# Performance work log

Measured on AMD Instinct MI355X. Metric: run time of the kernel, lower is better.

Reference implementation:

```python
import jax, jax.numpy as jnp
import numpy as np

B, T, D, U = 32, 1024, 512, 512

def hard_sigmoid(x):
    # Keras hard_sigmoid: clip(0.2*x + 0.5, 0, 1)
    return jnp.clip(x * 0.2 + 0.5, 0.0, 1.0)

def setup_inputs() -> dict:
    key = jax.random.key(0)
    k1, k2, k3 = jax.random.split(key, 3)
    x = jax.random.normal(k1, (B, T, D), dtype=jnp.float32)
    kernel = jax.random.normal(k2, (D, 4 * U), dtype=jnp.float32) * 0.02
    recurrent_kernel = jax.random.normal(k3, (U, 4 * U), dtype=jnp.float32) * 0.02
    # unit_forget_bias: forget-gate slice initialized to 1
    bias = jnp.zeros((4 * U,), dtype=jnp.float32).at[U:2 * U].set(1.0)
    return {"x": x, "kernel": kernel, "recurrent_kernel": recurrent_kernel, "bias": bias}

def reference(x, kernel, recurrent_kernel, bias):
    units = recurrent_kernel.shape[0]
    batch = x.shape[0]
    # Precompute input projections for all timesteps in one big GEMM
    # (implementation=2 style): [B, T, 4U]
    xz = jnp.einsum('btd,dg->btg', x, kernel) + bias
    xz_t = jnp.transpose(xz, (1, 0, 2))  # [T, B, 4U]

    h0 = jnp.zeros((batch, units), dtype=x.dtype)
    c0 = jnp.zeros((batch, units), dtype=x.dtype)

    def step(carry, z_x):
        h, c = carry
        z = z_x + h @ recurrent_kernel  # [B, 4U]
        zi, zf, zc, zo = jnp.split(z, 4, axis=-1)
        i = hard_sigmoid(zi)
        f = hard_sigmoid(zf)
        c_new = f * c + i * jnp.tanh(zc)
        o = hard_sigmoid(zo)
        h_new = o * jnp.tanh(c_new)
        return (h_new, c_new), h_new

    (_, _), hs = jax.lax.scan(step, (h0, c0), xz_t)  # hs: [T, B, U]
    return jnp.transpose(hs, (1, 0, 2))  # [B, T, U] (return_sequences=True)
```

## Files before the change

### kernel.cpp

```cpp
#include <hip/hip_runtime.h>


#define TT 1024
#define DD 512
#define UU 512
#define NCOL 2048
#define SENT 0xFFFFFFFFu
#define RDEPTH 4
#define SLOTS 4
#define WS_NEED 279552

typedef float f32x2 __attribute__((ext_vector_type(2)));
typedef float f32x4 __attribute__((ext_vector_type(4)));

__device__ __forceinline__ float hsig(float v) {
  return fminf(fmaxf(0.2f * v + 0.5f, 0.0f), 1.0f);
}
__device__ __forceinline__ float tanh_fast(float x) {
  float e = __expf(2.0f * x);
  return 1.0f - 2.0f / (e + 1.0f);
}

template <bool SLEEP>
__device__ __forceinline__ void wavebar(int* ctr, int& ep) {
  asm volatile("s_waitcnt lgkmcnt(0)" ::: "memory");
  if ((threadIdx.x & 63) == 0)
    __hip_atomic_fetch_add(ctr, 1, __ATOMIC_RELAXED, __HIP_MEMORY_SCOPE_WORKGROUP);
  ep += 4;
  while (__hip_atomic_load(ctr, __ATOMIC_RELAXED, __HIP_MEMORY_SCOPE_WORKGROUP) < ep) {
    if (SLEEP) __builtin_amdgcn_s_sleep(1);
  }
  asm volatile("" ::: "memory");
}

#define SENTSHOT(v0,v1,v2,v3,v4,v5,v6,v7,p0,p1,p2,p3)                    \
  asm volatile(                                                          \
      "global_load_dword %0, %8, off sc0 sc1\n\t"                        \
      "global_load_dword %1, %8, off offset:256 sc0 sc1\n\t"             \
      "global_load_dword %2, %9, off sc0 sc1\n\t"                        \
      "global_load_dword %3, %9, off offset:256 sc0 sc1\n\t"             \
      "global_load_dword %4, %10, off sc0 sc1\n\t"                       \
      "global_load_dword %5, %10, off offset:256 sc0 sc1\n\t"            \
      "global_load_dword %6, %11, off sc0 sc1\n\t"                       \
      "global_load_dword %7, %11, off offset:256 sc0 sc1\n\t"            \
      "s_waitcnt vmcnt(0)"                                               \
      : "=v"(v0), "=v"(v1), "=v"(v2), "=v"(v3),                          \
        "=v"(v4), "=v"(v5), "=v"(v6), "=v"(v7)                           \
      : "v"(p0), "v"(p1), "v"(p2), "v"(p3)                               \
      : "memory")

#define OK8(v0,v1,v2,v3,v4,v5,v6,v7)                                     \
  ((v0 != SENT) & (v1 != SENT) & (v2 != SENT) & (v3 != SENT) &           \
   (v4 != SENT) & (v5 != SENT) & (v6 != SENT) & (v7 != SENT))

__global__ __launch_bounds__(512, 2) void lstm_persistent(
    const float* __restrict__ x,
    const float* __restrict__ Wk,
    const float* __restrict__ Wr,
    const float* __restrict__ bias,
    float* __restrict__ out,
    int* __restrict__ wsbase) {
  const int tid = (int)threadIdx.x;
  const int g   = (int)blockIdx.x & 7;
  const int w   = (int)blockIdx.x >> 3;
  const bool crit = (tid < 256);
  const int l   = tid & 63;
  const bool has_ws = (wsbase != nullptr);

  int* tags   = wsbase;
  int* wscnt  = wsbase + 4096;
  int* wsmask = wsbase + 4104;
  float* fastH = (float*)wsbase + 4352;

  if (has_ws && tid == 0) {
    unsigned xcd;
    asm volatile("s_getreg_b32 %0, hwreg(HW_REG_XCC_ID)" : "=s"(xcd));
    __hip_atomic_fetch_or(wsmask + g, 1u << (xcd & 31), __ATOMIC_RELAXED,
                          __HIP_MEMORY_SCOPE_AGENT);
    __hip_atomic_fetch_add(wscnt + g, 1, __ATOMIC_RELEASE,
                           __HIP_MEMORY_SCOPE_AGENT);
  }

  __shared__ float LX[8][4][65];
  __shared__ float LR[2][8][4][66];
  __shared__ float RING[RDEPTH][4][66];
  __shared__ float LH[4][8][68];
  __shared__ float LB[64];
  __shared__ int cXZdone, cCRITdone, cXZbar, cCRITbar, sFast;

  if (tid == 0) { cXZdone = 0; cCRITdone = 0; cXZbar = 0; cCRITbar = 0; }
  if (tid < 64) LB[tid] = bias[(tid >> 4) * UU + w * 16 + (tid & 15)];

  f32x2 W2[64];
  {
    const int wv  = tid >> 6;
    const int idx = tid & 255;
    const int cp  = crit ? (l & 31) : (idx & 31);
    const int ko  = crit ? (2 * (wv & 3) + (l >> 5)) : (idx >> 5);
    const int gcb = (cp >> 3) * UU + w * 16 + ((2 * cp) & 15);
    const float* M = crit ? Wr : Wk;
#pragma unroll
    for (int j = 0; j < 64; ++j)
      W2[j] = *(const f32x2*)(M + (size_t)(64 * ko + j) * NCOL + gcb);
  }
  if (tid == 0) {
    int fast = 0;
    if (has_ws) {
      int ok = 0;
      for (int it = 0; it < 200000; ++it) {
        if (__hip_atomic_load(wscnt + g, __ATOMIC_ACQUIRE,
                              __HIP_MEMORY_SCOPE_AGENT) >= 32) { ok = 1; break; }
        __builtin_amdgcn_s_sleep(8);
      }
      if (ok) {
        unsigned m = (unsigned)__hip_atomic_load(wsmask + g, __ATOMIC_RELAXED,
                                                 __HIP_MEMORY_SCOPE_AGENT);
        fast = (__popc(m) == 1) ? 1 : 0;
      }
    }
    sFast = fast;
  }
  __syncthreads();
  const bool fastm = (sFast != 0);

  if (crit) {
    const int wv  = tid >> 6;
    const int kq0 = 2 * wv;
    const int kql = kq0 + (l >> 5);
    const int cp  = l & 31;
    const unsigned* ou0 = (const unsigned*)out + (size_t)(g * 4 + 0) * TT * UU;
    const unsigned* ou1 = (const unsigned*)out + (size_t)(g * 4 + 1) * TT * UU;
    const unsigned* ou2 = (const unsigned*)out + (size_t)(g * 4 + 2) * TT * UU;
    const unsigned* ou3 = (const unsigned*)out + (size_t)(g * 4 + 3) * TT * UU;
    float c_state = 0.0f;
    int epC = 0;

    for (int t = 0; t < TT; ++t) {
      if (t > 0) {
        const size_t roff = (size_t)(t - 1) * UU + 128 * wv + l;
        const unsigned* p0 = ou0 + roff;
        const unsigned* p1 = ou1 + roff;
        const unsigned* p2 = ou2 + roff;
        const unsigned* p3 = ou3 + roff;
        unsigned v0, v1, v2, v3, v4, v5, v6, v7;
        if (fastm) {
          const int slot = (t - 1) & (SLOTS - 1);
          const int* tp = tags +
              (((g * SLOTS + slot) * 32) + 8 * wv + (l & 7)) * 4 + ((l >> 3) & 3);
          const float* fb0 = fastH + ((size_t)((g * SLOTS + slot) * 4 + 0)) * 512 + 128 * wv + l;
          const float* fb1 = fastH + ((size_t)((g * SLOTS + slot) * 4 + 1)) * 512 + 128 * wv + l;
          const float* fb2 = fastH + ((size_t)((g * SLOTS + slot) * 4 + 2)) * 512 + 128 * wv + l;
          const float* fb3 = fastH + ((size_t)((g * SLOTS + slot) * 4 + 3)) * 512 + 128 * wv + l;
          int miss = 0;
          for (;;) {
            int tg;
            asm volatile("global_load_dword %0, %1, off sc0\n\ts_waitcnt vmcnt(0)"
                         : "=v"(tg) : "v"(tp) : "memory");
            if (__all(tg == t - 1)) {
              asm volatile(
                  "global_load_dword %0, %8, off sc0\n\t"
                  "global_load_dword %1, %8, off offset:256 sc0\n\t"
                  "global_load_dword %2, %9, off sc0\n\t"
                  "global_load_dword %3, %9, off offset:256 sc0\n\t"
                  "global_load_dword %4, %10, off sc0\n\t"
                  "global_load_dword %5, %10, off offset:256 sc0\n\t"
                  "global_load_dword %6, %11, off sc0\n\t"
                  "global_load_dword %7, %11, off offset:256 sc0\n\t"
                  "s_waitcnt vmcnt(0)"
                  : "=v"(v0), "=v"(v1), "=v"(v2), "=v"(v3),
                    "=v"(v4), "=v"(v5), "=v"(v6), "=v"(v7)
                  : "v"(fb0), "v"(fb1), "v"(fb2), "v"(fb3)
                  : "memory");
              break;
            }
            if (((++miss) & 7) == 0) {
              SENTSHOT(v0, v1, v2, v3, v4, v5, v6, v7, p0, p1, p2, p3);
              if (__all(OK8(v0, v1, v2, v3, v4, v5, v6, v7))) break;
            }
            __builtin_amdgcn_s_sleep(1);
          }
        } else {
          for (;;) {
            SENTSHOT(v0, v1, v2, v3, v4, v5, v6, v7, p0, p1, p2, p3);
            if (__all(OK8(v0, v1, v2, v3, v4, v5, v6, v7))) break;
            __builtin_amdgcn_s_sleep(16);
          }
        }
        LH[0][kq0    ][l] = __uint_as_float(v0);
        LH[0][kq0 + 1][l] = __uint_as_float(v1);
        LH[1][kq0    ][l] = __uint_as_float(v2);
        LH[1][kq0 + 1][l] = __uint_as_float(v3);
        LH[2][kq0    ][l] = __uint_as_float(v4);
        LH[2][kq0 + 1][l] = __uint_as_float(v5);
        LH[3][kq0    ][l] = __uint_as_float(v6);
        LH[3][kq0 + 1][l] = __uint_as_float(v7);
        asm volatile("s_waitcnt lgkmcnt(0)" ::: "memory");
        __builtin_amdgcn_sched_barrier(0);
        __builtin_amdgcn_s_setprio(1);
        f32x2 a0 = {0.f, 0.f}, a1 = {0.f, 0.f}, a2 = {0.f, 0.f}, a3 = {0.f, 0.f};
#pragma unroll
        for (int j4 = 0; j4 < 16; ++j4) {
          f32x4 h0 = *(const f32x4*)&LH[0][kql][4 * j4];
          f32x4 h1 = *(const f32x4*)&LH[1][kql][4 * j4];
          f32x4 h2 = *(const f32x4*)&LH[2][kql][4 * j4];
          f32x4 h3 = *(const f32x4*)&LH[3][kql][4 * j4];
#pragma unroll
          for (int jj = 0; jj < 4; ++jj) {
            f32x2 wj = W2[4 * j4 + jj];
            a0 += (f32x2){h0[jj], h0[jj]} * wj;
            a1 += (f32x2){h1[jj], h1[jj]} * wj;
            a2 += (f32x2){h2[jj], h2[jj]} * wj;
            a3 += (f32x2){h3[jj], h3[jj]} * wj;
          }
        }
        __builtin_amdgcn_s_setprio(0);
        const int p = t & 1;
        *(f32x2*)&LR[p][kql][0][2 * cp] = a0;
        *(f32x2*)&LR[p][kql][1][2 * cp] = a1;
        *(f32x2*)&LR[p][kql][2][2 * cp] = a2;
        *(f32x2*)&LR[p][kql][3][2 * cp] = a3;
      }
      float s0 = 0.f, s1 = 0.f, s2 = 0.f, s3 = 0.f;
      if (l < 16) {
        while (__hip_atomic_load(&cXZdone, __ATOMIC_RELAXED,
                                 __HIP_MEMORY_SCOPE_WORKGROUP) < t + 1) {
        }
        asm volatile("" ::: "memory");
        const int ss = t & (RDEPTH - 1);
        s0 = RING[ss][wv][l +  0] + LB[l +  0];
        s1 = RING[ss][wv][l + 16] + LB[l + 16];
        s2 = RING[ss][wv][l + 32] + LB[l + 32];
        s3 = RING[ss][wv][l + 48] + LB[l + 48];
      }
      wavebar<false>(&cCRITbar, epC);
      if (l == 0)
        __hip_atomic_fetch_add(&cCRITdone, 1, __ATOMIC_RELAXED,
                               __HIP_MEMORY_SCOPE_WORKGROUP);
      if (l < 16) {
        if (t > 0) {
          const int p = t & 1;
#pragma unroll
          for (int kq = 0; kq < 8; ++kq) {
            s0 += LR[p][kq][wv][l +  0];
            s1 += LR[p][kq][wv][l + 16];
            s2 += LR[p][kq][wv][l + 32];
            s3 += LR[p][kq][wv][l + 48];
          }
        }
        float gi = hsig(s0);
        float gf = hsig(s1);
        float gc = tanh_fast(s2);
        float go = hsig(s3);
        c_state = gf * c_state + gi * gc;
        float h = go * tanh_fast(c_state);
        if (fastm) {
          float* fp = fastH +
              ((size_t)((g * SLOTS + (t & (SLOTS - 1))) * 4 + wv)) * 512 + 16 * w + l;
          asm volatile("global_store_dword %0, %1, off sc0"
                       :: "v"(fp), "v"(h) : "memory");
          asm volatile("s_waitcnt vmcnt(0)" ::: "memory");
          if (l == 0) {
            int tv = t;
            int* tq = tags + (((g * SLOTS + (t & (SLOTS - 1))) * 32) + w) * 4 + wv;
            asm volatile("global_store_dword %0, %1, off sc0"
                         :: "v"(tq), "v"(tv) : "memory");
          }
        }
        __hip_atomic_store(
            out + ((size_t)(g * 4 + wv) * TT + t) * UU + w * 16 + l, h,
            __ATOMIC_RELAXED, __HIP_MEMORY_SCOPE_AGENT);
      }
    }
  } else {
    const int idx = tid & 255;
    const int o   = idx >> 5;
    const int cp  = idx & 31;
    const float* xb0 = x + (size_t)(g * 4 + 0) * TT * DD + o * 64;
    const float* xb1 = x + (size_t)(g * 4 + 1) * TT * DD + o * 64;
    const float* xb2 = x + (size_t)(g * 4 + 2) * TT * DD + o * 64;
    const float* xb3 = x + (size_t)(g * 4 + 3) * TT * DD + o * 64;
    int epX = 0;

    for (int t = 0; t < TT; ++t) {
      const size_t off = (size_t)t * DD;
      f32x2 a0 = {0.f, 0.f}, a1 = {0.f, 0.f}, a2 = {0.f, 0.f}, a3 = {0.f, 0.f};
#pragma unroll
      for (int j4 = 0; j4 < 16; ++j4) {
        f32x4 v0 = *(const f32x4*)(xb0 + off + 4 * j4);
        f32x4 v1 = *(const f32x4*)(xb1 + off + 4 * j4);
        f32x4 v2 = *(const f32x4*)(xb2 + off + 4 * j4);
        f32x4 v3 = *(const f32x4*)(xb3 + off + 4 * j4);
#pragma unroll
        for (int jj = 0; jj < 4; ++jj) {
          f32x2 wj = W2[4 * j4 + jj];
          a0 += (f32x2){v0[jj], v0[jj]} * wj;
          a1 += (f32x2){v1[jj], v1[jj]} * wj;
          a2 += (f32x2){v2[jj], v2[jj]} * wj;
          a3 += (f32x2){v3[jj], v3[jj]} * wj;
        }
      }
      *(f32x2*)&LX[o][0][2 * cp] = a0;
      *(f32x2*)&LX[o][1][2 * cp] = a1;
      *(f32x2*)&LX[o][2][2 * cp] = a2;
      *(f32x2*)&LX[o][3][2 * cp] = a3;
      wavebar<true>(&cXZbar, epX);
      if (t >= RDEPTH) {
        while (__hip_atomic_load(&cCRITdone, __ATOMIC_RELAXED,
                                 __HIP_MEMORY_SCOPE_WORKGROUP) <
               4 * (t - RDEPTH + 1)) {
          __builtin_amdgcn_s_sleep(1);
        }
        asm volatile("" ::: "memory");
      }
      {
        const int b2 = idx >> 6, c3 = idx & 63;
        float ssum = 0.f;
#pragma unroll
        for (int oo = 0; oo < 8; ++oo) ssum += LX[oo][b2][c3];
        RING[t & (RDEPTH - 1)][b2][c3] = ssum;
      }
      wavebar<true>(&cXZbar, epX);
      if (idx == 0) {
        asm volatile("s_waitcnt lgkmcnt(0)" ::: "memory");
        __hip_atomic_fetch_add(&cXZdone, 1, __ATOMIC_RELAXED,
                               __HIP_MEMORY_SCOPE_WORKGROUP);
      }
    }
  }
}

extern "C" void kernel_launch(void* const* d_in, const int* in_sizes, int n_in,
                              void* d_out, int out_size, void* d_ws, size_t ws_size,
                              hipStream_t stream) {
  const float* x    = (const float*)d_in[0];
  const float* Wk   = (const float*)d_in[1];
  const float* Wr   = (const float*)d_in[2];
  const float* bias = (const float*)d_in[3];
  float* out = (float*)d_out;

  int* wsbase = nullptr;
  if (ws_size >= (size_t)WS_NEED) {
    wsbase = (int*)d_ws;
    hipMemsetAsync(wsbase, 0xFF, 16384, stream);
    hipMemsetAsync((char*)d_ws + 16384, 0x00, 64, stream);
  }
  hipMemsetAsync(out, 0xFF, (size_t)out_size * sizeof(float), stream);
  lstm_persistent<<<256, 512, 0, stream>>>(x, Wk, Wr, bias, out, wsbase);
}
```

Baseline: 4.561 ms.

## Encode step parity into hidden-state values to drop separate tag flags

Replaces the tag-plus-data handshake for the fast hidden-state exchange with self-validating data. Each h value is stored offset by ±3, with the sign chosen by the step's colour bit, so the reader checks exponent and sign to confirm freshness and then subtracts the offset. This removes the tag store, the vmcnt wait before it, and the separate tag poll round-trip on the critical recurrence path. It adds a small rounding error from the ±3 add and subtract, relies on |h|<1 to keep the encoded exponent in range, and drops the ordering between data and tag writes.

```diff
diff --git a/kernel.cpp b/kernel.cpp
--- a/kernel.cpp
+++ b/kernel.cpp
@@ -7,8 +7,7 @@
 #define NCOL 2048
 #define SENT 0xFFFFFFFFu
 #define RDEPTH 4
-#define SLOTS 4
-#define WS_NEED 279552
+#define WS_NEED 263168
 
 typedef float f32x2 __attribute__((ext_vector_type(2)));
 typedef float f32x4 __attribute__((ext_vector_type(4)));
@@ -53,6 +52,11 @@
   ((v0 != SENT) & (v1 != SENT) & (v2 != SENT) & (v3 != SENT) &           \
    (v4 != SENT) & (v5 != SENT) & (v6 != SENT) & (v7 != SENT))
 
+__device__ __forceinline__ int encok(unsigned b, unsigned expsign) {
+  unsigned e = (b >> 23) & 0xFF;
+  return (int)(((e == 128u) | (e == 129u)) & ((b >> 31) == expsign));
+}
+
 __global__ __launch_bounds__(512, 2) void lstm_persistent(
     const float* __restrict__ x,
     const float* __restrict__ Wk,
@@ -67,10 +71,9 @@
   const int l   = tid & 63;
   const bool has_ws = (wsbase != nullptr);
 
-  int* tags   = wsbase;
-  int* wscnt  = wsbase + 4096;
-  int* wsmask = wsbase + 4104;
-  float* fastH = (float*)wsbase + 4352;
+  int* wscnt  = wsbase;
+  int* wsmask = wsbase + 8;
+  float* ring = (float*)wsbase + 256;
 
   if (has_ws && tid == 0) {
     unsigned xcd;
@@ -143,39 +146,65 @@
         const unsigned* p2 = ou2 + roff;
         const unsigned* p3 = ou3 + roff;
         unsigned v0, v1, v2, v3, v4, v5, v6, v7;
+        float h0v, h1v, h2v, h3v, h4v, h5v, h6v, h7v;
         if (fastm) {
-          const int slot = (t - 1) & (SLOTS - 1);
-          const int* tp = tags +
-              (((g * SLOTS + slot) * 32) + 8 * wv + (l & 7)) * 4 + ((l >> 3) & 3);
-          const float* fb0 = fastH + ((size_t)((g * SLOTS + slot) * 4 + 0)) * 512 + 128 * wv + l;
-          const float* fb1 = fastH + ((size_t)((g * SLOTS + slot) * 4 + 1)) * 512 + 128 * wv + l;
-          const float* fb2 = fastH + ((size_t)((g * SLOTS + slot) * 4 + 2)) * 512 + 128 * wv + l;
-          const float* fb3 = fastH + ((size_t)((g * SLOTS + slot) * 4 + 3)) * 512 + 128 * wv + l;
+          const int tau   = t - 1;
+          const int slot  = tau & 3;
+          const unsigned color = (unsigned)((tau >> 2) & 1);
+          const unsigned expsign = color ? 0u : 1u;
+          const float dec = color ? -3.0f : 3.0f;
+          const unsigned* fb0 = (const unsigned*)ring +
+              ((size_t)((g * 4 + slot) * 4 + 0)) * 512 + 128 * wv + l;
+          const unsigned* fb1 = (const unsigned*)ring +
+              ((size_t)((g * 4 + slot) * 4 + 1)) * 512 + 128 * wv + l;
+          const unsigned* fb2 = (const unsigned*)ring +
+              ((size_t)((g * 4 + slot) * 4 + 2)) * 512 + 128 * wv + l;
+          const unsigned* fb3 = (const unsigned*)ring +
+              ((size_t)((g * 4 + slot) * 4 + 3)) * 512 + 128 * wv + l;
           int miss = 0;
           for (;;) {
-            int tg;
-            asm volatile("global_load_dword %0, %1, off sc0\n\ts_waitcnt vmcnt(0)"
-                         : "=v"(tg) : "v"(tp) : "memory");
-            if (__all(tg == t - 1)) {
-              asm volatile(
-                  "global_load_dword %0, %8, off sc0\n\t"
-                  "global_load_dword %1, %8, off offset:256 sc0\n\t"
-                  "global_load_dword %2, %9, off sc0\n\t"
-                  "global_load_dword %3, %9, off offset:256 sc0\n\t"
-                  "global_load_dword %4, %10, off sc0\n\t"
-                  "global_load_dword %5, %10, off offset:256 sc0\n\t"
-                  "global_load_dword %6, %11, off sc0\n\t"
-                  "global_load_dword %7, %11, off offset:256 sc0\n\t"
-                  "s_waitcnt vmcnt(0)"
-                  : "=v"(v0), "=v"(v1), "=v"(v2), "=v"(v3),
-                    "=v"(v4), "=v"(v5), "=v"(v6), "=v"(v7)
-                  : "v"(fb0), "v"(fb1), "v"(fb2), "v"(fb3)
-                  : "memory");
+            asm volatile(
+                "global_load_dword %0, %8, off sc0\n\t"
+                "global_load_dword %1, %8, off offset:256 sc0\n\t"
+                "global_load_dword %2, %9, off sc0\n\t"
+                "global_load_dword %3, %9, off offset:256 sc0\n\t"
+                "global_load_dword %4, %10, off sc0\n\t"
+                "global_load_dword %5, %10, off offset:256 sc0\n\t"
+                "global_load_dword %6, %11, off sc0\n\t"
+                "global_load_dword %7, %11, off offset:256 sc0\n\t"
+                "s_waitcnt vmcnt(0)"
+                : "=v"(v0), "=v"(v1), "=v"(v2), "=v"(v3),
+                  "=v"(v4), "=v"(v5), "=v"(v6), "=v"(v7)
+                : "v"(fb0), "v"(fb1), "v"(fb2), "v"(fb3)
+                : "memory");
+            int ok = encok(v0, expsign) & encok(v1, expsign) &
+                     encok(v2, expsign) & encok(v3, expsign) &
+                     encok(v4, expsign) & encok(v5, expsign) &
+                     encok(v6, expsign) & encok(v7, expsign);
+            if (__all(ok)) {
+              h0v = __uint_as_float(v0) + dec;
+              h1v = __uint_as_float(v1) + dec;
+              h2v = __uint_as_float(v2) + dec;
+              h3v = __uint_as_float(v3) + dec;
+              h4v = __uint_as_float(v4) + dec;
+              h5v = __uint_as_float(v5) + dec;
+              h6v = __uint_as_float(v6) + dec;
+              h7v = __uint_as_float(v7) + dec;
               break;
             }
             if (((++miss) & 7) == 0) {
               SENTSHOT(v0, v1, v2, v3, v4, v5, v6, v7, p0, p1, p2, p3);
-              if (__all(OK8(v0, v1, v2, v3, v4, v5, v6, v7))) break;
+              if (__all(OK8(v0, v1, v2, v3, v4, v5, v6, v7))) {
+                h0v = __uint_as_float(v0);
+                h1v = __uint_as_float(v1);
+                h2v = __uint_as_float(v2);
+                h3v = __uint_as_float(v3);
+                h4v = __uint_as_float(v4);
+                h5v = __uint_as_float(v5);
+                h6v = __uint_as_float(v6);
+                h7v = __uint_as_float(v7);
+                break;
+              }
             }
             __builtin_amdgcn_s_sleep(1);
           }
@@ -185,15 +214,23 @@
             if (__all(OK8(v0, v1, v2, v3, v4, v5, v6, v7))) break;
             __builtin_amdgcn_s_sleep(16);
           }
-        }
-        LH[0][kq0    ][l] = __uint_as_float(v0);
-        LH[0][kq0 + 1][l] = __uint_as_float(v1);
-        LH[1][kq0    ][l] = __uint_as_float(v2);
-        LH[1][kq0 + 1][l] = __uint_as_float(v3);
-        LH[2][kq0    ][l] = __uint_as_float(v4);
-        LH[2][kq0 + 1][l] = __uint_as_float(v5);
-        LH[3][kq0    ][l] = __uint_as_float(v6);
-        LH[3][kq0 + 1][l] = __uint_as_float(v7);
+          h0v = __uint_as_float(v0);
+          h1v = __uint_as_float(v1);
+          h2v = __uint_as_float(v2);
+          h3v = __uint_as_float(v3);
+          h4v = __uint_as_float(v4);
+          h5v = __uint_as_float(v5);
+          h6v = __uint_as_float(v6);
+          h7v = __uint_as_float(v7);
+        }
+        LH[0][kq0    ][l] = h0v;
+        LH[0][kq0 + 1][l] = h1v;
+        LH[1][kq0    ][l] = h2v;
+        LH[1][kq0 + 1][l] = h3v;
+        LH[2][kq0    ][l] = h4v;
+        LH[2][kq0 + 1][l] = h5v;
+        LH[3][kq0    ][l] = h6v;
+        LH[3][kq0 + 1][l] = h7v;
         asm volatile("s_waitcnt lgkmcnt(0)" ::: "memory");
         __builtin_amdgcn_sched_barrier(0);
         __builtin_amdgcn_s_setprio(1);
@@ -254,17 +291,11 @@
         c_state = gf * c_state + gi * gc;
         float h = go * tanh_fast(c_state);
         if (fastm) {
-          float* fp = fastH +
-              ((size_t)((g * SLOTS + (t & (SLOTS - 1))) * 4 + wv)) * 512 + 16 * w + l;
+          const float enc = ((t >> 2) & 1) ? (h + 3.0f) : (h - 3.0f);
+          float* fp = ring +
+              ((size_t)((g * 4 + (t & 3)) * 4 + wv)) * 512 + 16 * w + l;
           asm volatile("global_store_dword %0, %1, off sc0"
-                       :: "v"(fp), "v"(h) : "memory");
-          asm volatile("s_waitcnt vmcnt(0)" ::: "memory");
-          if (l == 0) {
-            int tv = t;
-            int* tq = tags + (((g * SLOTS + (t & (SLOTS - 1))) * 32) + w) * 4 + wv;
-            asm volatile("global_store_dword %0, %1, off sc0"
-                         :: "v"(tq), "v"(tv) : "memory");
-          }
+                       :: "v"(fp), "v"(enc) : "memory");
         }
         __hip_atomic_store(
             out + ((size_t)(g * 4 + wv) * TT + t) * UU + w * 16 + l, h,
@@ -341,8 +372,8 @@
   int* wsbase = nullptr;
   if (ws_size >= (size_t)WS_NEED) {
     wsbase = (int*)d_ws;
-    hipMemsetAsync(wsbase, 0xFF, 16384, stream);
-    hipMemsetAsync((char*)d_ws + 16384, 0x00, 64, stream);
+    hipMemsetAsync(wsbase, 0x00, 64, stream);
+    hipMemsetAsync((char*)d_ws + 1024, 0xFF, 262144, stream);
   }
   hipMemsetAsync(out, 0xFF, (size_t)out_size * sizeof(float), stream);
   lstm_persistent<<<256, 512, 0, stream>>>(x, Wk, Wr, bias, out, wsbase);
```

Result: slower. 5.495 ms (+20.5%).
